# Kernel optimization log

Measured on AMD Instinct MI355X. Metric: run time of the kernel, lower is better.

The kernel has to match this reference:

```python
import jax, jax.numpy as jnp
import numpy as np

GAMMA = 267.52  # gyromagnetic ratio constant used as default in forward


def make_laplacian_kernel(vox=(1.0, 1.0, 1.0)):
    vx, vy, vz = vox
    mx, my, mz = 1.0 / vx ** 2, 1.0 / vy ** 2, 1.0 / vz ** 2
    mv = -2.0 * (mx + my + mz)
    k = np.zeros((3, 3, 3), dtype=np.float32)
    # layout matches the torch conv_op nested list: k[d, h, w]
    k[0, 1, 1] = mz
    k[2, 1, 1] = mz
    k[1, 0, 1] = mx
    k[1, 2, 1] = mx
    k[1, 1, 0] = my
    k[1, 1, 2] = my
    k[1, 1, 1] = mv
    return jnp.asarray(k)[None, None]  # [O=1, I=1, 3, 3, 3]


def lg(x, kernel):
    # conv3d, stride 1, padding 1 (SAME for 3^3 kernel), NCDHW
    out = jax.lax.conv_general_dilated(
        x, kernel, window_strides=(1, 1, 1), padding=[(1, 1)] * 3,
        dimension_numbers=('NCDHW', 'OIDHW', 'NCDHW'))
    # zero the boundary slices along each spatial dim (matches LG)
    out = out.at[:, :, 0, :, :].set(0.0).at[:, :, -1, :, :].set(0.0)
    out = out.at[:, :, :, 0, :].set(0.0).at[:, :, :, -1, :].set(0.0)
    out = out.at[:, :, :, :, 0].set(0.0).at[:, :, :, :, -1].set(0.0)
    return out


def setup_inputs() -> dict:
    key = jax.random.key(0)
    k1, k2 = jax.random.split(key)
    B, C, H, W, D = 2, 1, 256, 256, 128
    phi = jax.random.normal(k1, (B, C, H, W, D), dtype=jnp.float32)
    lfs = jax.random.normal(k2, (B, C, H, W, D), dtype=jnp.float32) * 0.01
    mask = jnp.ones((B, C, H, W, D), dtype=jnp.float32)
    TE = jax.random.uniform(jax.random.fold_in(key, 1), (B,), dtype=jnp.float32) * 0.02 + 0.005
    B0 = jnp.full((1,), 3.0, dtype=jnp.float32)
    kernel = make_laplacian_kernel((1.0, 1.0, 1.0))
    return {"phi": phi, "lfs": lfs, "mask": mask, "TE": TE, "B0": B0, "kernel": kernel}


def reference(phi, lfs, mask, TE, B0, kernel):
    expPhi_r = jnp.cos(phi)
    expPhi_i = jnp.sin(phi)
    a_r = lg(expPhi_r, kernel)
    a_i = lg(expPhi_i, kernel)
    b_i = (a_i * expPhi_r - a_r * expPhi_i) * mask
    te = TE[:, None, None, None, None]  # broadcast over [B,1,H,W,D]
    b_i = -b_i / (B0 * te * GAMMA)
    d_i = lg(lfs, kernel) * mask
    return (b_i, d_i)
```

## Files before the change

kernel.cpp:

```cpp
#include <hip/hip_runtime.h>

#define GAMMA_F 267.52f

typedef float v4f __attribute__((ext_vector_type(4)));

constexpr int H = 256, W = 256, D = 128;
constexpr int HS = 8;
constexpr long long sW = D;
constexpr long long sH = (long long)W * D;
constexpr long long sB = (long long)H * (long long)W * D;

__global__ __launch_bounds__(256) void lot_fused_hmarch(
    const float* __restrict__ phi,
    const float* __restrict__ lfs,
    const float* __restrict__ mask,
    const float* __restrict__ TE,
    const float* __restrict__ B0,
    const float* __restrict__ kern,
    float* __restrict__ out_b,
    float* __restrict__ out_d)
{
    const int tid = threadIdx.x;
    const int q   = tid & 31;
    const int wr  = tid >> 5;
    const int w   = blockIdx.x * 8 + wr;
    const int h0  = blockIdx.y * HS;
    const int b   = blockIdx.z;
    const int d0  = q * 4;

    const long long colBase = (long long)b * sB + (long long)w * sW + d0;

    if (w == 0 || w == W - 1) {
        const v4f z = {0.f, 0.f, 0.f, 0.f};
        #pragma unroll
        for (int i = 0; i < HS; ++i) {
            const long long r = colBase + (long long)(h0 + i) * sH;
            __builtin_nontemporal_store(z, (v4f*)(out_b + r));
            __builtin_nontemporal_store(z, (v4f*)(out_d + r));
        }
        return;
    }

    const float kHc = kern[4];
    const float kWc = kern[10];
    const float kDc = kern[12];
    const float kCc = kern[13];
    const float scale = -1.0f / (B0[0] * TE[b] * GAMMA_F);

    float Ps[3][6], Pc[3][6], Fl[3][6];

    #define LOAD_LINE(hh, SLOT)                                              \
    do {                                                                     \
        const int _h = (hh);                                                 \
        if (_h >= 0 && _h < H) {                                             \
            const long long _r = colBase + (long long)_h * sH;               \
            const v4f _p = *(const v4f*)(phi + _r);                          \
            const v4f _l = *(const v4f*)(lfs + _r);                          \
            float _t[6];                                                     \
            _t[1] = _p.x; _t[2] = _p.y; _t[3] = _p.z; _t[4] = _p.w;          \
            _t[0] = (d0 > 0)     ? phi[_r - 1] : 0.f;                        \
            _t[5] = (d0 + 4 < D) ? phi[_r + 4] : 0.f;                        \
            Fl[SLOT][1] = _l.x; Fl[SLOT][2] = _l.y;                          \
            Fl[SLOT][3] = _l.z; Fl[SLOT][4] = _l.w;                          \
            Fl[SLOT][0] = (d0 > 0)     ? lfs[_r - 1] : 0.f;                  \
            Fl[SLOT][5] = (d0 + 4 < D) ? lfs[_r + 4] : 0.f;                  \
            _Pragma("unroll")                                                \
            for (int _j = 0; _j < 6; ++_j) {                                 \
                Ps[SLOT][_j] = __sinf(_t[_j]);                               \
                Pc[SLOT][_j] = __cosf(_t[_j]);                               \
            }                                                                \
        } else {                                                             \
            _Pragma("unroll")                                                \
            for (int _j = 0; _j < 6; ++_j) {                                 \
                Ps[SLOT][_j] = 0.f; Pc[SLOT][_j] = 0.f; Fl[SLOT][_j] = 0.f;  \
            }                                                                \
        }                                                                    \
    } while (0)

    LOAD_LINE(h0 - 1, 0);
    LOAD_LINE(h0,     1);

    #pragma unroll
    for (int i = 0; i < HS; ++i) {
        const int h  = h0 + i;
        const int sm = i % 3;
        const int sc = (i + 1) % 3;
        const int sp = (i + 2) % 3;
        LOAD_LINE(h + 1, sp);

        const long long r = colBase + (long long)h * sH;
        if (h == 0 || h == H - 1) {
            const v4f z = {0.f, 0.f, 0.f, 0.f};
            __builtin_nontemporal_store(z, (v4f*)(out_b + r));
            __builtin_nontemporal_store(z, (v4f*)(out_d + r));
        } else {
            const v4f pw0 = *(const v4f*)(phi + r - sW);
            const v4f pw1 = *(const v4f*)(phi + r + sW);
            const v4f lw0 = *(const v4f*)(lfs + r - sW);
            const v4f lw1 = *(const v4f*)(lfs + r + sW);
            const v4f mk  = *(const v4f*)(mask + r);

            float sw0[4], cw0[4], sw1[4], cw1[4];
            {
                const float x0[4] = {pw0.x, pw0.y, pw0.z, pw0.w};
                const float x1[4] = {pw1.x, pw1.y, pw1.z, pw1.w};
                #pragma unroll
                for (int j = 0; j < 4; ++j) {
                    sw0[j] = __sinf(x0[j]); cw0[j] = __cosf(x0[j]);
                    sw1[j] = __sinf(x1[j]); cw1[j] = __cosf(x1[j]);
                }
            }
            const float lwv0[4] = {lw0.x, lw0.y, lw0.z, lw0.w};
            const float lwv1[4] = {lw1.x, lw1.y, lw1.z, lw1.w};
            const float mkv[4]  = {mk.x, mk.y, mk.z, mk.w};

            float ob[4], od[4];
            #pragma unroll
            for (int j = 0; j < 4; ++j) {
                const float se = Ps[sc][j + 1], ce = Pc[sc][j + 1];
                const float a_r = kCc * ce
                                + kDc * (Pc[sc][j] + Pc[sc][j + 2])
                                + kWc * (cw0[j] + cw1[j])
                                + kHc * (Pc[sm][j + 1] + Pc[sp][j + 1]);
                const float a_i = kCc * se
                                + kDc * (Ps[sc][j] + Ps[sc][j + 2])
                                + kWc * (sw0[j] + sw1[j])
                                + kHc * (Ps[sm][j + 1] + Ps[sp][j + 1]);
                float bi = (a_i * ce - a_r * se) * mkv[j] * scale;

                const float lap = kCc * Fl[sc][j + 1]
                                + kDc * (Fl[sc][j] + Fl[sc][j + 2])
                                + kWc * (lwv0[j] + lwv1[j])
                                + kHc * (Fl[sm][j + 1] + Fl[sp][j + 1]);
                float di = lap * mkv[j];

                const int d = d0 + j;
                if (d == 0 || d == D - 1) { bi = 0.f; di = 0.f; }
                ob[j] = bi; od[j] = di;
            }
            const v4f vb = {ob[0], ob[1], ob[2], ob[3]};
            const v4f vd = {od[0], od[1], od[2], od[3]};
            __builtin_nontemporal_store(vb, (v4f*)(out_b + r));
            __builtin_nontemporal_store(vd, (v4f*)(out_d + r));
        }
    }
    #undef LOAD_LINE
}

extern "C" void kernel_launch(void* const* d_in, const int* in_sizes, int n_in,
                              void* d_out, int out_size, void* d_ws, size_t ws_size,
                              hipStream_t stream) {
    const float* phi  = (const float*)d_in[0];
    const float* lfs  = (const float*)d_in[1];
    const float* mask = (const float*)d_in[2];
    const float* TE   = (const float*)d_in[3];
    const float* B0   = (const float*)d_in[4];
    const float* kern = (const float*)d_in[5];

    float* out_b = (float*)d_out;
    float* out_d = out_b + sB * 2;

    dim3 grid(W / 8, H / HS, 2);
    dim3 block(256);
    hipLaunchKernelGGL(lot_fused_hmarch, grid, block, 0, stream,
                       phi, lfs, mask, TE, B0, kern, out_b, out_d);
}
```

Baseline: 74.14 us.

## Share sin/cos of phi through LDS tiles instead of recomputing per thread

Each block now computes sin and cos of each phi value once for its 8-wide W tile plus halo columns. It writes them into a 3-slot ring buffer in shared memory and reads all stencil neighbours (D, W and H) from there. Before, each thread recomputed transcendentals for D-halo and W-neighbour values and reloaded the neighbouring phi columns. The H strip per block doubles to 16 rows, which reduces halo reloads, and the next row's phi is prefetched into registers. The cost is two __syncthreads per row and extra LDS traffic. Uninitialized LDS padding is read only for boundary outputs, which are then forced to zero.

Measured after the change: 66.94 us. 9.7% less time.

```diff
diff --git a/kernel.cpp b/kernel.cpp
--- a/kernel.cpp
+++ b/kernel.cpp
@@ -1,16 +1,18 @@
 #include <hip/hip_runtime.h>
 
 #define GAMMA_F 267.52f
-
 typedef float v4f __attribute__((ext_vector_type(4)));
 
 constexpr int H = 256, W = 256, D = 128;
-constexpr int HS = 8;
+constexpr int WT = 8;
+constexpr int HS = 16;
+constexpr int LW = WT + 2;
+constexpr int LD = D + 4;
 constexpr long long sW = D;
 constexpr long long sH = (long long)W * D;
 constexpr long long sB = (long long)H * (long long)W * D;
 
-__global__ __launch_bounds__(256) void lot_fused_hmarch(
+__global__ __launch_bounds__(256) void lot_lds_march(
     const float* __restrict__ phi,
     const float* __restrict__ lfs,
     const float* __restrict__ mask,
@@ -20,26 +22,20 @@
     float* __restrict__ out_b,
     float* __restrict__ out_d)
 {
+    __shared__ float Ssin[3][LW][LD];
+    __shared__ float Scos[3][LW][LD];
+
     const int tid = threadIdx.x;
     const int q   = tid & 31;
     const int wr  = tid >> 5;
-    const int w   = blockIdx.x * 8 + wr;
+    const int w0  = blockIdx.x * WT;
     const int h0  = blockIdx.y * HS;
     const int b   = blockIdx.z;
+    const int w   = w0 + wr;
     const int d0  = q * 4;
+    const int lwc = wr + 1;
 
     const long long colBase = (long long)b * sB + (long long)w * sW + d0;
-
-    if (w == 0 || w == W - 1) {
-        const v4f z = {0.f, 0.f, 0.f, 0.f};
-        #pragma unroll
-        for (int i = 0; i < HS; ++i) {
-            const long long r = colBase + (long long)(h0 + i) * sH;
-            __builtin_nontemporal_store(z, (v4f*)(out_b + r));
-            __builtin_nontemporal_store(z, (v4f*)(out_d + r));
-        }
-        return;
-    }
 
     const float kHc = kern[4];
     const float kWc = kern[10];
@@ -47,69 +43,93 @@
     const float kCc = kern[13];
     const float scale = -1.0f / (B0[0] * TE[b] * GAMMA_F);
 
-    float Ps[3][6], Pc[3][6], Fl[3][6];
+    const bool haloLo  = (wr == 0)      && (w0 > 0);
+    const bool haloHi  = (wr == WT - 1) && (w0 + WT < W);
+    const bool hasHalo = haloLo || haloHi;
+    const long long haloOff = haloLo ? -sW : sW;
+    const int  haloLw  = haloLo ? 0 : (LW - 1);
 
-    #define LOAD_LINE(hh, SLOT)                                              \
+    #define PHI_LOAD(hh, PREG, PHREG)                                        \
     do {                                                                     \
         const int _h = (hh);                                                 \
         if (_h >= 0 && _h < H) {                                             \
             const long long _r = colBase + (long long)_h * sH;               \
-            const v4f _p = *(const v4f*)(phi + _r);                          \
-            const v4f _l = *(const v4f*)(lfs + _r);                          \
-            float _t[6];                                                     \
-            _t[1] = _p.x; _t[2] = _p.y; _t[3] = _p.z; _t[4] = _p.w;          \
-            _t[0] = (d0 > 0)     ? phi[_r - 1] : 0.f;                        \
-            _t[5] = (d0 + 4 < D) ? phi[_r + 4] : 0.f;                        \
-            Fl[SLOT][1] = _l.x; Fl[SLOT][2] = _l.y;                          \
-            Fl[SLOT][3] = _l.z; Fl[SLOT][4] = _l.w;                          \
-            Fl[SLOT][0] = (d0 > 0)     ? lfs[_r - 1] : 0.f;                  \
-            Fl[SLOT][5] = (d0 + 4 < D) ? lfs[_r + 4] : 0.f;                  \
-            _Pragma("unroll")                                                \
-            for (int _j = 0; _j < 6; ++_j) {                                 \
-                Ps[SLOT][_j] = __sinf(_t[_j]);                               \
-                Pc[SLOT][_j] = __cosf(_t[_j]);                               \
-            }                                                                \
-        } else {                                                             \
-            _Pragma("unroll")                                                \
-            for (int _j = 0; _j < 6; ++_j) {                                 \
-                Ps[SLOT][_j] = 0.f; Pc[SLOT][_j] = 0.f; Fl[SLOT][_j] = 0.f;  \
-            }                                                                \
+            PREG = *(const v4f*)(phi + _r);                                  \
+            if (hasHalo) PHREG = *(const v4f*)(phi + _r + haloOff);          \
         }                                                                    \
     } while (0)
 
-    LOAD_LINE(h0 - 1, 0);
-    LOAD_LINE(h0,     1);
+    #define PHI_STORE(SLOT, PREG, PHREG)                                     \
+    do {                                                                     \
+        const int _s = (SLOT);                                               \
+        Ssin[_s][lwc][d0 + 1] = __sinf(PREG.x);                              \
+        Ssin[_s][lwc][d0 + 2] = __sinf(PREG.y);                              \
+        Ssin[_s][lwc][d0 + 3] = __sinf(PREG.z);                              \
+        Ssin[_s][lwc][d0 + 4] = __sinf(PREG.w);                              \
+        Scos[_s][lwc][d0 + 1] = __cosf(PREG.x);                              \
+        Scos[_s][lwc][d0 + 2] = __cosf(PREG.y);                              \
+        Scos[_s][lwc][d0 + 3] = __cosf(PREG.z);                              \
+        Scos[_s][lwc][d0 + 4] = __cosf(PREG.w);                              \
+        if (hasHalo) {                                                       \
+            Ssin[_s][haloLw][d0 + 1] = __sinf(PHREG.x);                      \
+            Ssin[_s][haloLw][d0 + 2] = __sinf(PHREG.y);                      \
+            Ssin[_s][haloLw][d0 + 3] = __sinf(PHREG.z);                      \
+            Ssin[_s][haloLw][d0 + 4] = __sinf(PHREG.w);                      \
+            Scos[_s][haloLw][d0 + 1] = __cosf(PHREG.x);                      \
+            Scos[_s][haloLw][d0 + 2] = __cosf(PHREG.y);                      \
+            Scos[_s][haloLw][d0 + 3] = __cosf(PHREG.z);                      \
+            Scos[_s][haloLw][d0 + 4] = __cosf(PHREG.w);                      \
+        }                                                                    \
+    } while (0)
 
-    #pragma unroll
+    #define LFS_LOAD(hh, F)                                                  \
+    do {                                                                     \
+        const int _h = (hh);                                                 \
+        if (_h >= 0 && _h < H) {                                             \
+            const long long _r = colBase + (long long)_h * sH;               \
+            const v4f _l = *(const v4f*)(lfs + _r);                          \
+            F[1] = _l.x; F[2] = _l.y; F[3] = _l.z; F[4] = _l.w;              \
+            F[0] = (d0 > 0)     ? lfs[_r - 1] : 0.f;                         \
+            F[5] = (d0 + 4 < D) ? lfs[_r + 4] : 0.f;                         \
+        } else {                                                             \
+            _Pragma("unroll")                                                \
+            for (int _j = 0; _j < 6; ++_j) F[_j] = 0.f;                      \
+        }                                                                    \
+    } while (0)
+
+    float FlA[6], FlB[6], FlC[6];
+    v4f pT = {0.f, 0.f, 0.f, 0.f}, pTH = {0.f, 0.f, 0.f, 0.f};
+
+    PHI_LOAD(h0 - 1, pT, pTH);
+    PHI_STORE(0, pT, pTH);
+    PHI_LOAD(h0, pT, pTH);
+    PHI_STORE(1, pT, pTH);
+    LFS_LOAD(h0 - 1, FlA);
+    LFS_LOAD(h0,     FlB);
+    v4f pN = pT, pNH = pTH;
+    PHI_LOAD(h0 + 1, pN, pNH);
+
+    int sm = 0, sc = 1, sp = 2;
+
     for (int i = 0; i < HS; ++i) {
-        const int h  = h0 + i;
-        const int sm = i % 3;
-        const int sc = (i + 1) % 3;
-        const int sp = (i + 2) % 3;
-        LOAD_LINE(h + 1, sp);
+        const int h = h0 + i;
+
+        PHI_STORE(sp, pN, pNH);
+        LFS_LOAD(h + 1, FlC);
+        __syncthreads();
+
+        v4f pN2 = pN, pN2H = pNH;
+        PHI_LOAD(h + 2, pN2, pN2H);
 
         const long long r = colBase + (long long)h * sH;
-        if (h == 0 || h == H - 1) {
+        if (h == 0 || h == H - 1 || w == 0 || w == W - 1) {
             const v4f z = {0.f, 0.f, 0.f, 0.f};
             __builtin_nontemporal_store(z, (v4f*)(out_b + r));
             __builtin_nontemporal_store(z, (v4f*)(out_d + r));
         } else {
-            const v4f pw0 = *(const v4f*)(phi + r - sW);
-            const v4f pw1 = *(const v4f*)(phi + r + sW);
             const v4f lw0 = *(const v4f*)(lfs + r - sW);
             const v4f lw1 = *(const v4f*)(lfs + r + sW);
             const v4f mk  = *(const v4f*)(mask + r);
-
-            float sw0[4], cw0[4], sw1[4], cw1[4];
-            {
-                const float x0[4] = {pw0.x, pw0.y, pw0.z, pw0.w};
-                const float x1[4] = {pw1.x, pw1.y, pw1.z, pw1.w};
-                #pragma unroll
-                for (int j = 0; j < 4; ++j) {
-                    sw0[j] = __sinf(x0[j]); cw0[j] = __cosf(x0[j]);
-                    sw1[j] = __sinf(x1[j]); cw1[j] = __cosf(x1[j]);
-                }
-            }
             const float lwv0[4] = {lw0.x, lw0.y, lw0.z, lw0.w};
             const float lwv1[4] = {lw1.x, lw1.y, lw1.z, lw1.w};
             const float mkv[4]  = {mk.x, mk.y, mk.z, mk.w};
@@ -117,34 +137,46 @@
             float ob[4], od[4];
             #pragma unroll
             for (int j = 0; j < 4; ++j) {
-                const float se = Ps[sc][j + 1], ce = Pc[sc][j + 1];
+                const int di = d0 + 1 + j;
+                const float se = Ssin[sc][lwc][di];
+                const float ce = Scos[sc][lwc][di];
                 const float a_r = kCc * ce
-                                + kDc * (Pc[sc][j] + Pc[sc][j + 2])
-                                + kWc * (cw0[j] + cw1[j])
-                                + kHc * (Pc[sm][j + 1] + Pc[sp][j + 1]);
+                    + kDc * (Scos[sc][lwc][di - 1] + Scos[sc][lwc][di + 1])
+                    + kWc * (Scos[sc][lwc - 1][di] + Scos[sc][lwc + 1][di])
+                    + kHc * (Scos[sm][lwc][di]     + Scos[sp][lwc][di]);
                 const float a_i = kCc * se
-                                + kDc * (Ps[sc][j] + Ps[sc][j + 2])
-                                + kWc * (sw0[j] + sw1[j])
-                                + kHc * (Ps[sm][j + 1] + Ps[sp][j + 1]);
+                    + kDc * (Ssin[sc][lwc][di - 1] + Ssin[sc][lwc][di + 1])
+                    + kWc * (Ssin[sc][lwc - 1][di] + Ssin[sc][lwc + 1][di])
+                    + kHc * (Ssin[sm][lwc][di]     + Ssin[sp][lwc][di]);
                 float bi = (a_i * ce - a_r * se) * mkv[j] * scale;
 
-                const float lap = kCc * Fl[sc][j + 1]
-                                + kDc * (Fl[sc][j] + Fl[sc][j + 2])
-                                + kWc * (lwv0[j] + lwv1[j])
-                                + kHc * (Fl[sm][j + 1] + Fl[sp][j + 1]);
-                float di = lap * mkv[j];
+                const float lap = kCc * FlB[j + 1]
+                    + kDc * (FlB[j] + FlB[j + 2])
+                    + kWc * (lwv0[j] + lwv1[j])
+                    + kHc * (FlA[j + 1] + FlC[j + 1]);
+                float dv = lap * mkv[j];
 
                 const int d = d0 + j;
-                if (d == 0 || d == D - 1) { bi = 0.f; di = 0.f; }
-                ob[j] = bi; od[j] = di;
+                if (d == 0 || d == D - 1) { bi = 0.f; dv = 0.f; }
+                ob[j] = bi; od[j] = dv;
             }
             const v4f vb = {ob[0], ob[1], ob[2], ob[3]};
             const v4f vd = {od[0], od[1], od[2], od[3]};
             __builtin_nontemporal_store(vb, (v4f*)(out_b + r));
             __builtin_nontemporal_store(vd, (v4f*)(out_d + r));
         }
+
+        pN = pN2; pNH = pN2H;
+        #pragma unroll
+        for (int j2 = 0; j2 < 6; ++j2) { FlA[j2] = FlB[j2]; FlB[j2] = FlC[j2]; }
+        const int t = sm; sm = sc; sc = sp; sp = t;
+
+        __syncthreads();
     }
-    #undef LOAD_LINE
+
+    #undef PHI_LOAD
+    #undef PHI_STORE
+    #undef LFS_LOAD
 }
 
 extern "C" void kernel_launch(void* const* d_in, const int* in_sizes, int n_in,
@@ -160,8 +192,8 @@
     float* out_b = (float*)d_out;
     float* out_d = out_b + sB * 2;
 
-    dim3 grid(W / 8, H / HS, 2);
+    dim3 grid(W / WT, H / HS, 2);
     dim3 block(256);
-    hipLaunchKernelGGL(lot_fused_hmarch, grid, block, 0, stream,
+    hipLaunchKernelGGL(lot_lds_march, grid, block, 0, stream,
                        phi, lfs, mask, TE, B0, kern, out_b, out_d);
 }
```

## Use sine-of-difference identity and warp shuffles for Laplacian phase term

Applied to the files above, without the earlier changes.

Rewrites the phase-Laplacian term as a sum of sin(neighbor - center), removing all cosine evaluations and the per-neighbor sin/cos pairs. Keeps raw phi/lfs rows in a register ring instead of precomputed sin/cos arrays, and obtains d-neighbors via warp shuffles rather than extra scalar loads. Adds an occupancy hint to launch bounds. Reduces transcendental work and register pressure, at the cost of relying on the boundary zeroing to mask padding differences.

Result: slower. 77.21 us (+4.1%).

```diff
diff --git a/kernel.cpp b/kernel.cpp
--- a/kernel.cpp
+++ b/kernel.cpp
@@ -1,16 +1,16 @@
 #include <hip/hip_runtime.h>
 
 #define GAMMA_F 267.52f
-
 typedef float v4f __attribute__((ext_vector_type(4)));
 
 constexpr int H = 256, W = 256, D = 128;
+constexpr int WT = 8;
 constexpr int HS = 8;
 constexpr long long sW = D;
 constexpr long long sH = (long long)W * D;
 constexpr long long sB = (long long)H * (long long)W * D;
 
-__global__ __launch_bounds__(256) void lot_fused_hmarch(
+__global__ __launch_bounds__(256, 4) void lot_sindiff(
     const float* __restrict__ phi,
     const float* __restrict__ lfs,
     const float* __restrict__ mask,
@@ -23,7 +23,7 @@
     const int tid = threadIdx.x;
     const int q   = tid & 31;
     const int wr  = tid >> 5;
-    const int w   = blockIdx.x * 8 + wr;
+    const int w   = blockIdx.x * WT + wr;
     const int h0  = blockIdx.y * HS;
     const int b   = blockIdx.z;
     const int d0  = q * 4;
@@ -47,104 +47,88 @@
     const float kCc = kern[13];
     const float scale = -1.0f / (B0[0] * TE[b] * GAMMA_F);
 
-    float Ps[3][6], Pc[3][6], Fl[3][6];
-
-    #define LOAD_LINE(hh, SLOT)                                              \
+    #define LD4(ptr, hh, DST)                                                \
     do {                                                                     \
         const int _h = (hh);                                                 \
         if (_h >= 0 && _h < H) {                                             \
-            const long long _r = colBase + (long long)_h * sH;               \
-            const v4f _p = *(const v4f*)(phi + _r);                          \
-            const v4f _l = *(const v4f*)(lfs + _r);                          \
-            float _t[6];                                                     \
-            _t[1] = _p.x; _t[2] = _p.y; _t[3] = _p.z; _t[4] = _p.w;          \
-            _t[0] = (d0 > 0)     ? phi[_r - 1] : 0.f;                        \
-            _t[5] = (d0 + 4 < D) ? phi[_r + 4] : 0.f;                        \
-            Fl[SLOT][1] = _l.x; Fl[SLOT][2] = _l.y;                          \
-            Fl[SLOT][3] = _l.z; Fl[SLOT][4] = _l.w;                          \
-            Fl[SLOT][0] = (d0 > 0)     ? lfs[_r - 1] : 0.f;                  \
-            Fl[SLOT][5] = (d0 + 4 < D) ? lfs[_r + 4] : 0.f;                  \
-            _Pragma("unroll")                                                \
-            for (int _j = 0; _j < 6; ++_j) {                                 \
-                Ps[SLOT][_j] = __sinf(_t[_j]);                               \
-                Pc[SLOT][_j] = __cosf(_t[_j]);                               \
-            }                                                                \
+            DST = *(const v4f*)((ptr) + colBase + (long long)_h * sH);       \
         } else {                                                             \
-            _Pragma("unroll")                                                \
-            for (int _j = 0; _j < 6; ++_j) {                                 \
-                Ps[SLOT][_j] = 0.f; Pc[SLOT][_j] = 0.f; Fl[SLOT][_j] = 0.f;  \
-            }                                                                \
+            DST = (v4f){0.f, 0.f, 0.f, 0.f};                                 \
         }                                                                    \
     } while (0)
 
-    LOAD_LINE(h0 - 1, 0);
-    LOAD_LINE(h0,     1);
+    v4f Pm, Pc, Pp, Lm, Lc, Lp;
+    LD4(phi, h0 - 1, Pm); LD4(phi, h0, Pc); LD4(phi, h0 + 1, Pp);
+    LD4(lfs, h0 - 1, Lm); LD4(lfs, h0, Lc); LD4(lfs, h0 + 1, Lp);
 
     #pragma unroll
     for (int i = 0; i < HS; ++i) {
-        const int h  = h0 + i;
-        const int sm = i % 3;
-        const int sc = (i + 1) % 3;
-        const int sp = (i + 2) % 3;
-        LOAD_LINE(h + 1, sp);
+        const int h = h0 + i;
+        const long long r = colBase + (long long)h * sH;
 
-        const long long r = colBase + (long long)h * sH;
+        v4f Pn, Ln;
+        LD4(phi, h + 2, Pn);
+        LD4(lfs, h + 2, Ln);
+
         if (h == 0 || h == H - 1) {
             const v4f z = {0.f, 0.f, 0.f, 0.f};
             __builtin_nontemporal_store(z, (v4f*)(out_b + r));
             __builtin_nontemporal_store(z, (v4f*)(out_d + r));
         } else {
-            const v4f pw0 = *(const v4f*)(phi + r - sW);
-            const v4f pw1 = *(const v4f*)(phi + r + sW);
-            const v4f lw0 = *(const v4f*)(lfs + r - sW);
-            const v4f lw1 = *(const v4f*)(lfs + r + sW);
-            const v4f mk  = *(const v4f*)(mask + r);
+            const v4f PwM = *(const v4f*)(phi + r - sW);
+            const v4f PwP = *(const v4f*)(phi + r + sW);
+            const v4f LwM = *(const v4f*)(lfs + r - sW);
+            const v4f LwP = *(const v4f*)(lfs + r + sW);
+            const v4f MK  = *(const v4f*)(mask + r);
 
-            float sw0[4], cw0[4], sw1[4], cw1[4];
-            {
-                const float x0[4] = {pw0.x, pw0.y, pw0.z, pw0.w};
-                const float x1[4] = {pw1.x, pw1.y, pw1.z, pw1.w};
-                #pragma unroll
-                for (int j = 0; j < 4; ++j) {
-                    sw0[j] = __sinf(x0[j]); cw0[j] = __cosf(x0[j]);
-                    sw1[j] = __sinf(x1[j]); cw1[j] = __cosf(x1[j]);
-                }
-            }
-            const float lwv0[4] = {lw0.x, lw0.y, lw0.z, lw0.w};
-            const float lwv1[4] = {lw1.x, lw1.y, lw1.z, lw1.w};
-            const float mkv[4]  = {mk.x, mk.y, mk.z, mk.w};
+            const float pdm = __shfl_up(Pc.w, 1, 32);
+            const float pdp = __shfl_down(Pc.x, 1, 32);
+            const float ldm = __shfl_up(Lc.w, 1, 32);
+            const float ldp = __shfl_down(Lc.x, 1, 32);
+
+            const float px[6]  = {pdm, Pc.x, Pc.y, Pc.z, Pc.w, pdp};
+            const float lx[6]  = {ldm, Lc.x, Lc.y, Lc.z, Lc.w, ldp};
+            const float pmv[4] = {Pm.x, Pm.y, Pm.z, Pm.w};
+            const float ppv[4] = {Pp.x, Pp.y, Pp.z, Pp.w};
+            const float lmv[4] = {Lm.x, Lm.y, Lm.z, Lm.w};
+            const float lpv[4] = {Lp.x, Lp.y, Lp.z, Lp.w};
+            const float pwm[4] = {PwM.x, PwM.y, PwM.z, PwM.w};
+            const float pwp[4] = {PwP.x, PwP.y, PwP.z, PwP.w};
+            const float lwm[4] = {LwM.x, LwM.y, LwM.z, LwM.w};
+            const float lwp[4] = {LwP.x, LwP.y, LwP.z, LwP.w};
+            const float mkv[4] = {MK.x, MK.y, MK.z, MK.w};
 
             float ob[4], od[4];
             #pragma unroll
             for (int j = 0; j < 4; ++j) {
-                const float se = Ps[sc][j + 1], ce = Pc[sc][j + 1];
-                const float a_r = kCc * ce
-                                + kDc * (Pc[sc][j] + Pc[sc][j + 2])
-                                + kWc * (cw0[j] + cw1[j])
-                                + kHc * (Pc[sm][j + 1] + Pc[sp][j + 1]);
-                const float a_i = kCc * se
-                                + kDc * (Ps[sc][j] + Ps[sc][j + 2])
-                                + kWc * (sw0[j] + sw1[j])
-                                + kHc * (Ps[sm][j + 1] + Ps[sp][j + 1]);
-                float bi = (a_i * ce - a_r * se) * mkv[j] * scale;
+                const float c = px[j + 1];
+                const float s =
+                      kDc * (__sinf(px[j]  - c) + __sinf(px[j + 2] - c))
+                    + kWc * (__sinf(pwm[j] - c) + __sinf(pwp[j]    - c))
+                    + kHc * (__sinf(pmv[j] - c) + __sinf(ppv[j]    - c));
+                float bi = s * mkv[j] * scale;
 
-                const float lap = kCc * Fl[sc][j + 1]
-                                + kDc * (Fl[sc][j] + Fl[sc][j + 2])
-                                + kWc * (lwv0[j] + lwv1[j])
-                                + kHc * (Fl[sm][j + 1] + Fl[sp][j + 1]);
-                float di = lap * mkv[j];
+                const float lap = kCc * lx[j + 1]
+                    + kDc * (lx[j] + lx[j + 2])
+                    + kWc * (lwm[j] + lwp[j])
+                    + kHc * (lmv[j] + lpv[j]);
+                float dv = lap * mkv[j];
 
                 const int d = d0 + j;
-                if (d == 0 || d == D - 1) { bi = 0.f; di = 0.f; }
-                ob[j] = bi; od[j] = di;
+                if (d == 0 || d == D - 1) { bi = 0.f; dv = 0.f; }
+                ob[j] = bi; od[j] = dv;
             }
             const v4f vb = {ob[0], ob[1], ob[2], ob[3]};
             const v4f vd = {od[0], od[1], od[2], od[3]};
             __builtin_nontemporal_store(vb, (v4f*)(out_b + r));
             __builtin_nontemporal_store(vd, (v4f*)(out_d + r));
         }
+
+        Pm = Pc; Pc = Pp; Pp = Pn;
+        Lm = Lc; Lc = Lp; Lp = Ln;
     }
-    #undef LOAD_LINE
+
+    #undef LD4
 }
 
 extern "C" void kernel_launch(void* const* d_in, const int* in_sizes, int n_in,
@@ -160,8 +144,8 @@
     float* out_b = (float*)d_out;
     float* out_d = out_b + sB * 2;
 
-    dim3 grid(W / 8, H / HS, 2);
+    dim3 grid(W / WT, H / HS, 2);
     dim3 block(256);
-    hipLaunchKernelGGL(lot_fused_hmarch, grid, block, 0, stream,
+    hipLaunchKernelGGL(lot_sindiff, grid, block, 0, stream,
                        phi, lfs, mask, TE, B0, kern, out_b, out_d);
 }
```
